# Performance work log

Hardware: AMD Instinct MI355X
Metric: run time of the kernel (lower is better)

Reference implementation:

```python
import jax, jax.numpy as jnp
import numpy as np
import math

EPS = 1e-8        # numeric guard in segment intersection (matches mmcv EPSILON)
MODE_EPS = 1e-6   # module's eps
N_BOXES = 1000000


def box2corners(box):
    # box: (B, N, 5) -> corners (B, N, 4, 2)
    cx, cy, w, h, a = [box[..., i:i + 1] for i in range(5)]
    x4 = jnp.asarray([0.5, -0.5, -0.5, 0.5], box.dtype) * w   # (B,N,4)
    y4 = jnp.asarray([-0.5, -0.5, 0.5, 0.5], box.dtype) * h
    c, s = jnp.cos(a), jnp.sin(a)
    return jnp.stack([x4 * c - y4 * s + cx, x4 * s + y4 * c + cy], axis=-1)


def box_intersection(corners1, corners2):
    # all pairwise segment intersections between edges of the two boxes
    line1 = jnp.concatenate([corners1, jnp.roll(corners1, -1, axis=2)], axis=-1)  # (B,N,4,4)
    line2 = jnp.concatenate([corners2, jnp.roll(corners2, -1, axis=2)], axis=-1)
    l1 = line1[:, :, :, None, :]  # (B,N,4,1,4)
    l2 = line2[:, :, None, :, :]  # (B,N,1,4,4)
    x1, y1, x2, y2 = l1[..., 0], l1[..., 1], l1[..., 2], l1[..., 3]
    x3, y3, x4, y4 = l2[..., 0], l2[..., 1], l2[..., 2], l2[..., 3]
    num = (y4 - y3) * (x2 - x1) - (x4 - x3) * (y2 - y1)
    den_t = (x4 - x3) * (y1 - y3) - (y4 - y3) * (x1 - x3)
    t = den_t / (num + EPS)
    t_chk = jnp.where(num == 0, -1.0, t)
    mask_t = (t_chk > 0) & (t_chk < 1)
    den_u = (x2 - x1) * (y1 - y3) - (y2 - y1) * (x1 - x3)
    u = -den_u / (num + EPS)
    u_chk = jnp.where(num == 0, -1.0, u)
    mask_u = (u_chk > 0) & (u_chk < 1)
    mask = mask_t & mask_u  # (B,N,4,4)
    pts = jnp.stack([x1 + t * (x2 - x1), y1 + t * (y2 - y1)], axis=-1)
    pts = pts * mask[..., None].astype(pts.dtype)
    return pts, mask  # (B,N,4,4,2), (B,N,4,4)


def box_in_box(corners1, corners2):
    # which corners of box1 lie inside box2 (projection test)
    a = corners2[:, :, 0:1, :]
    b = corners2[:, :, 1:2, :]
    d = corners2[:, :, 3:4, :]
    ab, ad, am = b - a, d - a, corners1 - a
    p_ab = jnp.sum(ab * am, -1) / jnp.sum(ab * ab, -1)
    p_ad = jnp.sum(ad * am, -1) / jnp.sum(ad * ad, -1)
    tol = 1e-6
    return (p_ab > -tol) & (p_ab < 1 + tol) & (p_ad > -tol) & (p_ad < 1 + tol)


def intersection_area(corners1, corners2):
    # differentiable convex-intersection area via vertex sort + shoelace
    inter_pts, inter_mask = box_intersection(corners1, corners2)
    c1_in_2 = box_in_box(corners1, corners2)
    c2_in_1 = box_in_box(corners2, corners1)
    B, N = corners1.shape[:2]
    verts = jnp.concatenate([corners1, corners2, inter_pts.reshape(B, N, 16, 2)], axis=2)  # (B,N,24,2)
    mask = jnp.concatenate([c1_in_2, c2_in_1, inter_mask.reshape(B, N, 16)], axis=2)       # (B,N,24)
    num_valid = jnp.sum(mask, axis=-1, keepdims=True).astype(verts.dtype)  # (B,N,1)
    center = jnp.sum(verts * mask[..., None], axis=2) / jnp.maximum(num_valid, 1.0)  # (B,N,2)
    v = verts - center[:, :, None, :]
    ang = jnp.where(mask, jnp.arctan2(v[..., 1], v[..., 0]), 1e7)  # invalid -> end
    order = jnp.argsort(ang, axis=-1)
    v_sorted = jnp.take_along_axis(v, order[..., None], axis=2)
    m_sorted = jnp.take_along_axis(mask, order, axis=2)
    first = v_sorted[:, :, 0:1, :]
    poly = jnp.where(m_sorted[..., None], v_sorted, first)  # pad with first vertex (closes polygon)
    nxt = jnp.roll(poly, -1, axis=2)
    cross = poly[..., 0] * nxt[..., 1] - poly[..., 1] * nxt[..., 0]
    return jnp.abs(jnp.sum(cross, axis=-1)) * 0.5  # (B,N)


def diff_iou_rotated_2d(box1, box2):
    c1, c2 = box2corners(box1), box2corners(box2)
    inter = intersection_area(c1, c2)
    area1 = box1[..., 2] * box1[..., 3]
    area2 = box2[..., 2] * box2[..., 3]
    return inter / (area1 + area2 - inter)


def obb2hbb_xyxy(obb):
    cx, cy, w, h, a = obb[:, 0], obb[:, 1], obb[:, 2], obb[:, 3], obb[:, 4]
    c, s = jnp.abs(jnp.cos(a)), jnp.abs(jnp.sin(a))
    dw = (w * c + h * s) * 0.5
    dh = (w * s + h * c) * 0.5
    return jnp.stack([cx - dw, cy - dh, cx + dw, cy + dh], axis=-1)


def setup_inputs():
    key = jax.random.key(0)
    k = jax.random.split(key, 7)
    N = N_BOXES
    cxy = jax.random.uniform(k[0], (N, 2), jnp.float32, 0.0, 1024.0)
    wh = jax.random.uniform(k[1], (N, 2), jnp.float32, 8.0, 128.0)
    ang = jax.random.uniform(k[2], (N, 1), jnp.float32, -np.pi / 2, np.pi / 2)
    pred = jnp.concatenate([cxy, wh, ang], axis=-1)
    jit_xy = jax.random.uniform(k[3], (N, 2), jnp.float32, -10.0, 10.0)
    jit_wh = jax.random.uniform(k[4], (N, 2), jnp.float32, 0.8, 1.25)
    jit_a = jax.random.uniform(k[5], (N, 1), jnp.float32, -0.3, 0.3)
    target = jnp.concatenate([pred[:, :2] + jit_xy, pred[:, 2:4] * jit_wh, pred[:, 4:5] + jit_a], axis=-1)
    weight = jax.random.uniform(k[6], (N,), jnp.float32, 0.5, 1.5)
    return {"pred": pred, "target": target, "weight": weight}


def reference(pred, target, weight):
    eps = MODE_EPS
    ious = jnp.clip(diff_iou_rotated_2d(pred[None], target[None])[0], 0.0, 1.0)  # (N,)
    # enclosing HBB for penalty terms
    hp, ht = obb2hbb_xyxy(pred), obb2hbb_xyxy(target)
    en_wh = jnp.clip(jnp.maximum(hp[:, 2:], ht[:, 2:]) - jnp.minimum(hp[:, :2], ht[:, :2]), 0.0)
    c2 = en_wh[:, 0] ** 2 + en_wh[:, 1] ** 2 + eps
    rho2 = (target[:, 0] - pred[:, 0]) ** 2 + (target[:, 1] - pred[:, 1]) ** 2
    factor = 4.0 / (math.pi ** 2)
    v = factor * (jnp.arctan(target[:, 2] / (target[:, 3] + eps)) - jnp.arctan(pred[:, 2] / (pred[:, 3] + eps))) ** 2
    alpha = jax.lax.stop_gradient((ious > 0.5).astype(v.dtype) * v / (1.0 - ious + v + eps))
    cious = ious - (jnp.clip(rho2 / c2, 0.0, 1.0) + alpha * v)
    loss = (1.0 - cious) * weight
    return jnp.mean(loss)  # loss_weight=1.0, reduction='mean'
```

## Files before the change

### kernel.cpp

```cpp
#include <hip/hip_runtime.h>
#include <math.h>


#define BLOCK 256
#define NV 16
#define PAIRS 2
#define LDS_STRIDE 17

typedef float v2f __attribute__((ext_vector_type(2)));

struct CEList {
    int n;
    unsigned char lo[128];
    unsigned char hi[128];
};

constexpr CEList make_ces16() {
    CEList L{};
    L.n = 0;
    for (int p = 1; p < NV; p <<= 1)
        for (int k = p; k >= 1; k >>= 1)
            for (int j = k % p; j + k < NV; j += 2 * k)
                for (int i = 0; i < k; i++) {
                    int lo = i + j, hi = i + j + k;
                    if (hi < NV && (lo / (2 * p)) == (hi / (2 * p))) {
                        L.lo[L.n] = (unsigned char)lo;
                        L.hi[L.n] = (unsigned char)hi;
                        L.n++;
                    }
                }
    return L;
}

constexpr CEList CES = make_ces16();

__device__ __forceinline__ float frcp(float x) {
    return __builtin_amdgcn_rcpf(x);
}

__device__ __forceinline__ v2f splat2(float x) {
    v2f r; r.x = x; r.y = x; return r;
}

__device__ __forceinline__ float hadd2(v2f v) { return v.x + v.y; }

__device__ __forceinline__ float angle_key(float x, float y) {
    float ax = fabsf(x), ay = fabsf(y);
    float den = ax + ay;
    float r = x * frcp(den);
    r = (den > 0.f) ? r : 0.f;
    return (y >= 0.f) ? (1.f - r) : (3.f + r);
}

__device__ __forceinline__ unsigned int pack_bf2(float x, float y) {
    unsigned int bx = __float_as_uint(x) + 0x8000u;
    unsigned int by = __float_as_uint(y) + 0x8000u;
    return (by & 0xFFFF0000u) | (bx >> 16);
}

__device__ __forceinline__ float atan01(float z) {
    float z2 = z * z;
    float p = -0.01172120f;
    p = p * z2 + 0.05265332f;
    p = p * z2 - 0.11643287f;
    p = p * z2 + 0.19354346f;
    p = p * z2 - 0.33262347f;
    p = p * z2 + 0.99997726f;
    return z * p;
}

__device__ __forceinline__ float pair_loss(const float* __restrict__ p,
                                           const float* __restrict__ t,
                                           float wv,
                                           unsigned int* __restrict__ myb)
{
    const float EPSf  = 1e-8f;
    const float TOLf  = 1e-6f;
    const float MEPS  = 1e-6f;
    const float PIf   = 3.14159265358979323846f;

    float pcx = p[0], pcy = p[1], pw = p[2], ph = p[3], pa = p[4];
    float tcx = t[0], tcy = t[1], tw = t[2], th = t[3], ta = t[4];

    float ca = __cosf(pa), sa = __sinf(pa);
    float cb = __cosf(ta), sb = __sinf(ta);
    v2f C1[4], C2[4];
    {
        const float xs[4] = { 0.5f, -0.5f, -0.5f, 0.5f };
        const float ys[4] = { -0.5f, -0.5f, 0.5f, 0.5f };
        v2f R1x = { ca, sa },  R1y = { -sa, cb };
        R1y.x = -sa; R1y.y = ca;
        v2f R2x = { cb, sb },  R2y = { -sb, cb };
        R2y.x = -sb; R2y.y = cb;
        v2f CT1 = { pcx, pcy }, CT2 = { tcx, tcy };
        #pragma unroll
        for (int k = 0; k < 4; k++) {
            float x4 = xs[k] * pw, y4 = ys[k] * ph;
            C1[k] = splat2(x4) * R1x + splat2(y4) * R1y + CT1;
            float x4b = xs[k] * tw, y4b = ys[k] * th;
            C2[k] = splat2(x4b) * R2x + splat2(y4b) * R2y + CT2;
        }
    }

    v2f  V[NV];
    bool msk[NV];

    {
        v2f A  = C2[0];
        v2f AB = C2[1] - A, AD = C2[3] - A;
        float rab = frcp(hadd2(AB * AB));
        float rad = frcp(hadd2(AD * AD));
        #pragma unroll
        for (int k = 0; k < 4; k++) {
            v2f AM = C1[k] - A;
            float pab = hadd2(AB * AM) * rab;
            float pad = hadd2(AD * AM) * rad;
            msk[k] = (pab > -TOLf) && (pab < 1.f + TOLf) &&
                     (pad > -TOLf) && (pad < 1.f + TOLf);
            V[k] = C1[k];
        }
    }
    {
        v2f A  = C1[0];
        v2f AB = C1[1] - A, AD = C1[3] - A;
        float rab = frcp(hadd2(AB * AB));
        float rad = frcp(hadd2(AD * AD));
        #pragma unroll
        for (int k = 0; k < 4; k++) {
            v2f AM = C2[k] - A;
            float pab = hadd2(AB * AM) * rab;
            float pad = hadd2(AD * AM) * rad;
            msk[4 + k] = (pab > -TOLf) && (pab < 1.f + TOLf) &&
                         (pad > -TOLf) && (pad < 1.f + TOLf);
            V[4 + k] = C2[k];
        }
    }
    #pragma unroll
    for (int e1 = 0; e1 < 4; e1++) {
        v2f P1 = C1[e1];
        v2f E  = C1[(e1 + 1) & 3] - P1;
        v2f  Q[4];
        bool qm[4];
        #pragma unroll
        for (int e2 = 0; e2 < 4; e2++) {
            v2f P3 = C2[e2];
            v2f F  = C2[(e2 + 1) & 3] - P3;
            float num  = F.y * E.x - F.x * E.y;
            float rnum = frcp(num + EPSf);
            v2f D = P1 - P3;
            float den_t = F.x * D.y - F.y * D.x;
            float den_u = E.x * D.y - E.y * D.x;
            float tt = den_t * rnum;
            float uu = -den_u * rnum;
            qm[e2] = (num != 0.f) && (tt > 0.f) && (tt < 1.f)
                                  && (uu > 0.f) && (uu < 1.f);
            Q[e2] = splat2(tt) * E + P1;
        }
        bool mfL = qm[0] || qm[1];
        v2f  fL  = qm[0] ? Q[0] : Q[1];
        bool msL = qm[0] && qm[1];
        bool mfR = qm[2] || qm[3];
        v2f  fR  = qm[2] ? Q[2] : Q[3];
        bool msR = qm[2] && qm[3];
        int s0 = 8 + 2 * e1, s1 = s0 + 1;
        V[s0]   = mfL ? fL : fR;
        msk[s0] = mfL || mfR;
        v2f  t2 = msL ? Q[1] : fR;
        V[s1]   = mfL ? t2 : Q[3];
        msk[s1] = msL || (mfL && mfR) || msR;
    }

    v2f s2 = { 0.f, 0.f };
    float cnt = 0.f;
    const v2f Z2 = { 0.f, 0.f };
    #pragma unroll
    for (int k = 0; k < NV; k++) {
        s2  += msk[k] ? V[k] : Z2;
        cnt += msk[k] ? 1.f : 0.f;
    }
    float rden = frcp(fmaxf(cnt, 1.f));
    v2f cen = s2 * splat2(rden);

    unsigned int ku[NV];
    #pragma unroll
    for (int k = 0; k < NV; k++) {
        v2f R = V[k] - cen;
        myb[k] = pack_bf2(R.x, R.y);
        float a = msk[k] ? angle_key(R.x, R.y) : 1e7f;
        ku[k] = (__float_as_uint(a) & 0xFFFFFFF0u) | (unsigned int)k;
    }

    #pragma unroll
    for (int c = 0; c < CES.n; c++) {
        const int lo = CES.lo[c], hi = CES.hi[c];
        unsigned int a = ku[lo], b = ku[hi];
        ku[lo] = a < b ? a : b;
        ku[hi] = a < b ? b : a;
    }

    const unsigned int VALID_LIM = 0x49742400u;
    float gx[NV], gy[NV];
    bool  gv[NV];
    #pragma unroll
    for (int k = 0; k < NV; k++) {
        unsigned int pk = myb[ku[k] & 15u];
        gx[k] = __uint_as_float(pk << 16);
        gy[k] = __uint_as_float(pk & 0xFFFF0000u);
        gv[k] = ku[k] < VALID_LIM;
    }
    float fx = gx[0], fy = gy[0];
    float cross = 0.f;
    #pragma unroll
    for (int k = 0; k < NV; k++) {
        int kn = (k + 1) % NV;
        float axv = gv[k]  ? gx[k]  : fx, ayv = gv[k]  ? gy[k]  : fy;
        float bxv = gv[kn] ? gx[kn] : fx, byv = gv[kn] ? gy[kn] : fy;
        cross += axv * byv - ayv * bxv;
    }
    float inter = fabsf(cross) * 0.5f;

    float area1 = pw * ph, area2 = tw * th;
    float iou = inter * frcp(area1 + area2 - inter);
    iou = fminf(fmaxf(iou, 0.f), 1.f);

    float cA = fabsf(ca), sA = fabsf(sa);
    float cB = fabsf(cb), sB = fabsf(sb);
    float dw1 = (pw * cA + ph * sA) * 0.5f, dh1 = (pw * sA + ph * cA) * 0.5f;
    float dw2 = (tw * cB + th * sB) * 0.5f, dh2 = (tw * sB + th * cB) * 0.5f;
    float hp0 = pcx - dw1, hp1 = pcy - dh1, hp2 = pcx + dw1, hp3 = pcy + dh1;
    float ht0 = tcx - dw2, ht1 = tcy - dh2, ht2 = tcx + dw2, ht3 = tcy + dh2;

    float enw = fmaxf(fmaxf(hp2, ht2) - fminf(hp0, ht0), 0.f);
    float enh = fmaxf(fmaxf(hp3, ht3) - fminf(hp1, ht1), 0.f);
    float c2v = enw * enw + enh * enh + MEPS;
    float rho2 = (tcx - pcx) * (tcx - pcx) + (tcy - pcy) * (tcy - pcy);

    float factor = 4.f / (PIf * PIf);
    float r1 = tw * frcp(th + MEPS);
    float r2 = pw * frcp(ph + MEPS);
    float xd = (r1 - r2) * frcp(1.f + r1 * r2);
    float axd = fabsf(xd);
    bool  big = axd > 1.f;
    float z   = big ? frcp(axd) : axd;
    float at  = atan01(z);
    float dv  = big ? ((0.5f * PIf) - at) : at;
    float v_ = factor * dv * dv;
    float alpha = (iou > 0.5f) ? v_ * frcp(1.f - iou + v_ + MEPS) : 0.f;

    float rhoterm = fminf(fmaxf(rho2 * frcp(c2v), 0.f), 1.f);
    float ciou = iou - (rhoterm + alpha * v_);
    return (1.f - ciou) * wv;
}

__global__ __launch_bounds__(BLOCK)
void obb_ciou_kernel(const float* __restrict__ pred,
                     const float* __restrict__ tgt,
                     const float* __restrict__ wgt,
                     float* __restrict__ out,
                     int N, float invN)
{
    __shared__ unsigned int slab[BLOCK * LDS_STRIDE];
    unsigned int* myb = slab + (int)threadIdx.x * LDS_STRIDE;

    int blk0 = blockIdx.x * (BLOCK * PAIRS);
    float loss = 0.f;

    #pragma unroll
    for (int u = 0; u < PAIRS; u++) {
        int i = blk0 + u * BLOCK + (int)threadIdx.x;
        if (i < N)
            loss += pair_loss(pred + (size_t)i * 5, tgt + (size_t)i * 5,
                              wgt[i], myb);
    }

    #pragma unroll
    for (int off = 32; off > 0; off >>= 1)
        loss += __shfl_down(loss, off, 64);

    __shared__ float red[BLOCK / 64];
    int wave = threadIdx.x >> 6;
    int lane = threadIdx.x & 63;
    if (lane == 0) red[wave] = loss;
    __syncthreads();
    if (threadIdx.x == 0) {
        float s = 0.f;
        #pragma unroll
        for (int w = 0; w < BLOCK / 64; w++) s += red[w];
        atomicAdd(out, s * invN);
    }
}

extern "C" void kernel_launch(void* const* d_in, const int* in_sizes, int n_in,
                              void* d_out, int out_size, void* d_ws, size_t ws_size,
                              hipStream_t stream) {
    const float* pred = (const float*)d_in[0];
    const float* tgt  = (const float*)d_in[1];
    const float* wgt  = (const float*)d_in[2];
    float* out = (float*)d_out;
    int N = in_sizes[2];

    hipMemsetAsync(out, 0, sizeof(float) * (size_t)out_size, stream);

    int grid = (N + BLOCK * PAIRS - 1) / (BLOCK * PAIRS);
    obb_ciou_kernel<<<grid, BLOCK, 0, stream>>>(pred, tgt, wgt, out, N,
                                                1.f / (float)N);
}
```

Measured before the change: 108.0 us.

## Compute intersection in pred box frame and interleave two pairs per thread

Rewrites the polygon construction in the predicted box's local frame, so box1 is axis-aligned. This turns point-in-box tests into abs comparisons and edge intersections into a single division per edge pair. It also interleaves the two pairs per thread for ILP, gives each pair its own LDS slab, and sets launch bounds to 4 blocks per CU. The trade-offs are higher register pressure and a doubled LDS footprint per block, and the changed tolerance handling could shift edge-case results slightly.

```diff
diff --git a/kernel.cpp b/kernel.cpp
--- a/kernel.cpp
+++ b/kernel.cpp
@@ -3,8 +3,8 @@
 
 
 #define BLOCK 256
+#define PAIRS 2
 #define NV 16
-#define PAIRS 2
 #define LDS_STRIDE 17
 
 typedef float v2f __attribute__((ext_vector_type(2)));
@@ -42,7 +42,10 @@
     v2f r; r.x = x; r.y = x; return r;
 }
 
-__device__ __forceinline__ float hadd2(v2f v) { return v.x + v.y; }
+__device__ __forceinline__ v2f rot_ds(v2f e, float cd, float sd) {
+    v2f sw; sw.x = e.y; sw.y = -e.x;
+    return e * splat2(cd) + sw * splat2(sd);
+}
 
 __device__ __forceinline__ float angle_key(float x, float y) {
     float ax = fabsf(x), ay = fabsf(y);
@@ -69,208 +72,275 @@
     return z * p;
 }
 
-__device__ __forceinline__ float pair_loss(const float* __restrict__ p,
-                                           const float* __restrict__ t,
-                                           float wv,
-                                           unsigned int* __restrict__ myb)
-{
-    const float EPSf  = 1e-8f;
-    const float TOLf  = 1e-6f;
-    const float MEPS  = 1e-6f;
-    const float PIf   = 3.14159265358979323846f;
-
-    float pcx = p[0], pcy = p[1], pw = p[2], ph = p[3], pa = p[4];
-    float tcx = t[0], tcy = t[1], tw = t[2], th = t[3], ta = t[4];
-
-    float ca = __cosf(pa), sa = __sinf(pa);
-    float cb = __cosf(ta), sb = __sinf(ta);
-    v2f C1[4], C2[4];
-    {
-        const float xs[4] = { 0.5f, -0.5f, -0.5f, 0.5f };
-        const float ys[4] = { -0.5f, -0.5f, 0.5f, 0.5f };
-        v2f R1x = { ca, sa },  R1y = { -sa, cb };
-        R1y.x = -sa; R1y.y = ca;
-        v2f R2x = { cb, sb },  R2y = { -sb, cb };
-        R2y.x = -sb; R2y.y = cb;
-        v2f CT1 = { pcx, pcy }, CT2 = { tcx, tcy };
-        #pragma unroll
-        for (int k = 0; k < 4; k++) {
-            float x4 = xs[k] * pw, y4 = ys[k] * ph;
-            C1[k] = splat2(x4) * R1x + splat2(y4) * R1y + CT1;
-            float x4b = xs[k] * tw, y4b = ys[k] * th;
-            C2[k] = splat2(x4b) * R2x + splat2(y4b) * R2y + CT2;
-        }
-    }
-
-    v2f  V[NV];
-    bool msk[NV];
-
-    {
-        v2f A  = C2[0];
-        v2f AB = C2[1] - A, AD = C2[3] - A;
-        float rab = frcp(hadd2(AB * AB));
-        float rad = frcp(hadd2(AD * AD));
-        #pragma unroll
-        for (int k = 0; k < 4; k++) {
-            v2f AM = C1[k] - A;
-            float pab = hadd2(AB * AM) * rab;
-            float pad = hadd2(AD * AM) * rad;
-            msk[k] = (pab > -TOLf) && (pab < 1.f + TOLf) &&
-                     (pad > -TOLf) && (pad < 1.f + TOLf);
-            V[k] = C1[k];
-        }
-    }
-    {
-        v2f A  = C1[0];
-        v2f AB = C1[1] - A, AD = C1[3] - A;
-        float rab = frcp(hadd2(AB * AB));
-        float rad = frcp(hadd2(AD * AD));
-        #pragma unroll
-        for (int k = 0; k < 4; k++) {
-            v2f AM = C2[k] - A;
-            float pab = hadd2(AB * AM) * rab;
-            float pad = hadd2(AD * AM) * rad;
-            msk[4 + k] = (pab > -TOLf) && (pab < 1.f + TOLf) &&
-                         (pad > -TOLf) && (pad < 1.f + TOLf);
-            V[4 + k] = C2[k];
-        }
-    }
-    #pragma unroll
-    for (int e1 = 0; e1 < 4; e1++) {
-        v2f P1 = C1[e1];
-        v2f E  = C1[(e1 + 1) & 3] - P1;
-        v2f  Q[4];
-        bool qm[4];
-        #pragma unroll
-        for (int e2 = 0; e2 < 4; e2++) {
-            v2f P3 = C2[e2];
-            v2f F  = C2[(e2 + 1) & 3] - P3;
-            float num  = F.y * E.x - F.x * E.y;
-            float rnum = frcp(num + EPSf);
-            v2f D = P1 - P3;
-            float den_t = F.x * D.y - F.y * D.x;
-            float den_u = E.x * D.y - E.y * D.x;
-            float tt = den_t * rnum;
-            float uu = -den_u * rnum;
-            qm[e2] = (num != 0.f) && (tt > 0.f) && (tt < 1.f)
-                                  && (uu > 0.f) && (uu < 1.f);
-            Q[e2] = splat2(tt) * E + P1;
-        }
-        bool mfL = qm[0] || qm[1];
-        v2f  fL  = qm[0] ? Q[0] : Q[1];
-        bool msL = qm[0] && qm[1];
-        bool mfR = qm[2] || qm[3];
-        v2f  fR  = qm[2] ? Q[2] : Q[3];
-        bool msR = qm[2] && qm[3];
-        int s0 = 8 + 2 * e1, s1 = s0 + 1;
-        V[s0]   = mfL ? fL : fR;
-        msk[s0] = mfL || mfR;
-        v2f  t2 = msL ? Q[1] : fR;
-        V[s1]   = mfL ? t2 : Q[3];
-        msk[s1] = msL || (mfL && mfR) || msR;
-    }
-
-    v2f s2 = { 0.f, 0.f };
-    float cnt = 0.f;
-    const v2f Z2 = { 0.f, 0.f };
-    #pragma unroll
-    for (int k = 0; k < NV; k++) {
-        s2  += msk[k] ? V[k] : Z2;
-        cnt += msk[k] ? 1.f : 0.f;
-    }
-    float rden = frcp(fmaxf(cnt, 1.f));
-    v2f cen = s2 * splat2(rden);
-
-    unsigned int ku[NV];
-    #pragma unroll
-    for (int k = 0; k < NV; k++) {
-        v2f R = V[k] - cen;
-        myb[k] = pack_bf2(R.x, R.y);
-        float a = msk[k] ? angle_key(R.x, R.y) : 1e7f;
-        ku[k] = (__float_as_uint(a) & 0xFFFFFFF0u) | (unsigned int)k;
-    }
-
-    #pragma unroll
-    for (int c = 0; c < CES.n; c++) {
-        const int lo = CES.lo[c], hi = CES.hi[c];
-        unsigned int a = ku[lo], b = ku[hi];
-        ku[lo] = a < b ? a : b;
-        ku[hi] = a < b ? b : a;
-    }
-
-    const unsigned int VALID_LIM = 0x49742400u;
-    float gx[NV], gy[NV];
-    bool  gv[NV];
-    #pragma unroll
-    for (int k = 0; k < NV; k++) {
-        unsigned int pk = myb[ku[k] & 15u];
-        gx[k] = __uint_as_float(pk << 16);
-        gy[k] = __uint_as_float(pk & 0xFFFF0000u);
-        gv[k] = ku[k] < VALID_LIM;
-    }
-    float fx = gx[0], fy = gy[0];
-    float cross = 0.f;
-    #pragma unroll
-    for (int k = 0; k < NV; k++) {
-        int kn = (k + 1) % NV;
-        float axv = gv[k]  ? gx[k]  : fx, ayv = gv[k]  ? gy[k]  : fy;
-        float bxv = gv[kn] ? gx[kn] : fx, byv = gv[kn] ? gy[kn] : fy;
-        cross += axv * byv - ayv * bxv;
-    }
-    float inter = fabsf(cross) * 0.5f;
-
-    float area1 = pw * ph, area2 = tw * th;
-    float iou = inter * frcp(area1 + area2 - inter);
-    iou = fminf(fmaxf(iou, 0.f), 1.f);
-
-    float cA = fabsf(ca), sA = fabsf(sa);
-    float cB = fabsf(cb), sB = fabsf(sb);
-    float dw1 = (pw * cA + ph * sA) * 0.5f, dh1 = (pw * sA + ph * cA) * 0.5f;
-    float dw2 = (tw * cB + th * sB) * 0.5f, dh2 = (tw * sB + th * cB) * 0.5f;
-    float hp0 = pcx - dw1, hp1 = pcy - dh1, hp2 = pcx + dw1, hp3 = pcy + dh1;
-    float ht0 = tcx - dw2, ht1 = tcy - dh2, ht2 = tcx + dw2, ht3 = tcy + dh2;
-
-    float enw = fmaxf(fmaxf(hp2, ht2) - fminf(hp0, ht0), 0.f);
-    float enh = fmaxf(fmaxf(hp3, ht3) - fminf(hp1, ht1), 0.f);
-    float c2v = enw * enw + enh * enh + MEPS;
-    float rho2 = (tcx - pcx) * (tcx - pcx) + (tcy - pcy) * (tcy - pcy);
-
-    float factor = 4.f / (PIf * PIf);
-    float r1 = tw * frcp(th + MEPS);
-    float r2 = pw * frcp(ph + MEPS);
-    float xd = (r1 - r2) * frcp(1.f + r1 * r2);
-    float axd = fabsf(xd);
-    bool  big = axd > 1.f;
-    float z   = big ? frcp(axd) : axd;
-    float at  = atan01(z);
-    float dv  = big ? ((0.5f * PIf) - at) : at;
-    float v_ = factor * dv * dv;
-    float alpha = (iou > 0.5f) ? v_ * frcp(1.f - iou + v_ + MEPS) : 0.f;
-
-    float rhoterm = fminf(fmaxf(rho2 * frcp(c2v), 0.f), 1.f);
-    float ciou = iou - (rhoterm + alpha * v_);
-    return (1.f - ciou) * wv;
-}
-
-__global__ __launch_bounds__(BLOCK)
+__global__ __launch_bounds__(BLOCK, 4)
 void obb_ciou_kernel(const float* __restrict__ pred,
                      const float* __restrict__ tgt,
                      const float* __restrict__ wgt,
                      float* __restrict__ out,
                      int N, float invN)
 {
-    __shared__ unsigned int slab[BLOCK * LDS_STRIDE];
-    unsigned int* myb = slab + (int)threadIdx.x * LDS_STRIDE;
-
-    int blk0 = blockIdx.x * (BLOCK * PAIRS);
+    const float MEPS = 1e-6f;
+    const float PIf  = 3.14159265358979323846f;
+    const float TOLm = 1.f + 2e-6f;
+
+    __shared__ unsigned int slab[PAIRS * BLOCK * LDS_STRIDE];
+    unsigned int* const mybp[2] = {
+        slab + (int)threadIdx.x * LDS_STRIDE,
+        slab + BLOCK * LDS_STRIDE + (int)threadIdx.x * LDS_STRIDE
+    };
+
+    int base = blockIdx.x * (BLOCK * PAIRS) + (int)threadIdx.x;
+
+    float pcx[2], pcy[2], pw[2], ph[2], pa[2];
+    float tcx[2], tcy[2], tw[2], th[2], ta[2];
+    float wv[2];
+    #pragma unroll
+    for (int u = 0; u < 2; u++) {
+        int i = base + u * BLOCK;
+        bool ok = i < N;
+        int ic = ok ? i : 0;
+        wv[u] = ok ? wgt[ic] : 0.f;
+        const float* p = pred + (size_t)ic * 5;
+        const float* t = tgt  + (size_t)ic * 5;
+        pcx[u] = p[0]; pcy[u] = p[1]; pw[u] = p[2]; ph[u] = p[3]; pa[u] = p[4];
+        tcx[u] = t[0]; tcy[u] = t[1]; tw[u] = t[2]; th[u] = t[3]; ta[u] = t[4];
+    }
+
+    float ca[2], sa[2], cb[2], sb[2];
+    float hw1[2], hh1[2], hw2[2], hh2[2];
+    float ddx[2], ddy[2], cd[2], sd[2];
+    v2f c2[2], A[2], B[2], C0[2], C1[2], C2c[2], C3[2];
+    #pragma unroll
+    for (int u = 0; u < 2; u++) {
+        ca[u] = __cosf(pa[u]); sa[u] = __sinf(pa[u]);
+        cb[u] = __cosf(ta[u]); sb[u] = __sinf(ta[u]);
+        hw1[u] = 0.5f * pw[u]; hh1[u] = 0.5f * ph[u];
+        hw2[u] = 0.5f * tw[u]; hh2[u] = 0.5f * th[u];
+        ddx[u] = tcx[u] - pcx[u]; ddy[u] = tcy[u] - pcy[u];
+        v2f dd;  dd.x = ddx[u];  dd.y = ddy[u];
+        v2f dds; dds.x = ddy[u]; dds.y = -ddx[u];
+        c2[u] = dd * splat2(ca[u]) + dds * splat2(sa[u]);
+        cd[u] = cb[u] * ca[u] + sb[u] * sa[u];
+        sd[u] = sb[u] * ca[u] - cb[u] * sa[u];
+        v2f axd2; axd2.x = cd[u];  axd2.y = sd[u];
+        v2f bxd2; bxd2.x = -sd[u]; bxd2.y = cd[u];
+        A[u] = splat2(hw2[u]) * axd2;
+        B[u] = splat2(hh2[u]) * bxd2;
+        v2f qpA = c2[u] + A[u], qmA = c2[u] - A[u];
+        C0[u] = qpA - B[u]; C1[u] = qmA - B[u];
+        C2c[u] = qmA + B[u]; C3[u] = qpA + B[u];
+    }
+
+    v2f  V[2][NV];
+    bool msk[2][NV];
+
+    {
+        float exl[2], exh[2], eyl[2], eyh[2], lw2[2], lh2[2];
+        #pragma unroll
+        for (int u = 0; u < 2; u++) {
+            exl[u] = -hw1[u] - c2[u].x; exh[u] = hw1[u] - c2[u].x;
+            eyl[u] = -hh1[u] - c2[u].y; eyh[u] = hh1[u] - c2[u].y;
+            lw2[u] = hw2[u] * TOLm; lh2[u] = hh2[u] * TOLm;
+        }
+        #pragma unroll
+        for (int k = 0; k < 4; k++) {
+            #pragma unroll
+            for (int u = 0; u < 2; u++) {
+                v2f e;
+                e.x = (k == 0 || k == 3) ? exh[u] : exl[u];
+                e.y = (k < 2) ? eyl[u] : eyh[u];
+                v2f duv = rot_ds(e, cd[u], sd[u]);
+                msk[u][k] = (fabsf(duv.x) < lw2[u]) && (fabsf(duv.y) < lh2[u]);
+                V[u][k].x = (k == 0 || k == 3) ? hw1[u] : -hw1[u];
+                V[u][k].y = (k < 2) ? -hh1[u] : hh1[u];
+            }
+        }
+    }
+
+    #pragma unroll
+    for (int u = 0; u < 2; u++) {
+        float lw1 = hw1[u] * TOLm, lh1 = hh1[u] * TOLm;
+        msk[u][4] = (fabsf(C0[u].x) < lw1) && (fabsf(C0[u].y) < lh1);
+        V[u][4] = C0[u];
+        msk[u][5] = (fabsf(C1[u].x) < lw1) && (fabsf(C1[u].y) < lh1);
+        V[u][5] = C1[u];
+        msk[u][6] = (fabsf(C2c[u].x) < lw1) && (fabsf(C2c[u].y) < lh1);
+        V[u][6] = C2c[u];
+        msk[u][7] = (fabsf(C3[u].x) < lw1) && (fabsf(C3[u].y) < lh1);
+        V[u][7] = C3[u];
+    }
+
+    {
+        float Sx[2][4], Sy[2][4], Dxe[2][4], Dye[2][4], iDx[2][4], iDy[2][4];
+        #pragma unroll
+        for (int u = 0; u < 2; u++) {
+            float twcd = A[u].x + A[u].x, twsd = A[u].y + A[u].y;
+            float thsd = -(B[u].x + B[u].x), thcd = B[u].y + B[u].y;
+            float rax = frcp(twcd), ray = frcp(twsd);
+            float rbx = frcp(thsd), rby = frcp(thcd);
+            Sx[u][0] = C0[u].x; Sx[u][1] = C1[u].x;
+            Sx[u][2] = C2c[u].x; Sx[u][3] = C3[u].x;
+            Sy[u][0] = C0[u].y; Sy[u][1] = C1[u].y;
+            Sy[u][2] = C2c[u].y; Sy[u][3] = C3[u].y;
+            Dxe[u][0] = -twcd; Dxe[u][1] = -thsd; Dxe[u][2] = twcd; Dxe[u][3] = thsd;
+            Dye[u][0] = -twsd; Dye[u][1] = thcd;  Dye[u][2] = twsd; Dye[u][3] = -thcd;
+            iDx[u][0] = -rax; iDx[u][1] = -rbx; iDx[u][2] = rax; iDx[u][3] = rbx;
+            iDy[u][0] = -ray; iDy[u][1] = rby;  iDy[u][2] = ray; iDy[u][3] = -rby;
+        }
+        #pragma unroll
+        for (int e1 = 0; e1 < 4; e1++) {
+            const bool horiz = (e1 == 0) || (e1 == 2);
+            float q[2][4]; bool qm[2][4];
+            #pragma unroll
+            for (int j = 0; j < 4; j++) {
+                #pragma unroll
+                for (int u = 0; u < 2; u++) {
+                    float cc  = (e1 == 0) ? -hh1[u] : (e1 == 1) ? -hw1[u]
+                              : (e1 == 2) ?  hh1[u] :  hw1[u];
+                    float lim = horiz ? hw1[u] : hh1[u];
+                    float uu = horiz ? (cc - Sy[u][j]) * iDy[u][j]
+                                     : (cc - Sx[u][j]) * iDx[u][j];
+                    float w = horiz ? fmaf(uu, Dxe[u][j], Sx[u][j])
+                                    : fmaf(uu, Dye[u][j], Sy[u][j]);
+                    qm[u][j] = (uu > -1.f) && (uu < 0.f) && (fabsf(w) < lim);
+                    q[u][j] = w;
+                }
+            }
+            #pragma unroll
+            for (int u = 0; u < 2; u++) {
+                float cc  = (e1 == 0) ? -hh1[u] : (e1 == 1) ? -hw1[u]
+                          : (e1 == 2) ?  hh1[u] :  hw1[u];
+                bool mfL = qm[u][0] || qm[u][1];
+                float fL = qm[u][0] ? q[u][0] : q[u][1];
+                bool msL = qm[u][0] && qm[u][1];
+                bool mfR = qm[u][2] || qm[u][3];
+                float fR = qm[u][2] ? q[u][2] : q[u][3];
+                bool msR = qm[u][2] && qm[u][3];
+                int s0 = 8 + 2 * e1, s1 = s0 + 1;
+                float w0 = mfL ? fL : fR;
+                msk[u][s0] = mfL || mfR;
+                float t2v = msL ? q[u][1] : fR;
+                float w1 = mfL ? t2v : q[u][3];
+                msk[u][s1] = msL || (mfL && mfR) || msR;
+                if (horiz) { V[u][s0].x = w0; V[u][s0].y = cc;
+                             V[u][s1].x = w1; V[u][s1].y = cc; }
+                else       { V[u][s0].x = cc; V[u][s0].y = w0;
+                             V[u][s1].x = cc; V[u][s1].y = w1; }
+            }
+        }
+    }
+
+    v2f s2[2]; float cnt[2];
+    #pragma unroll
+    for (int u = 0; u < 2; u++) { s2[u] = splat2(0.f); cnt[u] = 0.f; }
+    const v2f Z2 = splat2(0.f);
+    #pragma unroll
+    for (int k = 0; k < NV; k++) {
+        #pragma unroll
+        for (int u = 0; u < 2; u++) {
+            s2[u]  += msk[u][k] ? V[u][k] : Z2;
+            cnt[u] += msk[u][k] ? 1.f : 0.f;
+        }
+    }
+    v2f cen[2];
+    #pragma unroll
+    for (int u = 0; u < 2; u++)
+        cen[u] = s2[u] * splat2(frcp(fmaxf(cnt[u], 1.f)));
+
+    unsigned int ku[2][NV];
+    #pragma unroll
+    for (int k = 0; k < NV; k++) {
+        #pragma unroll
+        for (int u = 0; u < 2; u++) {
+            v2f R = V[u][k] - cen[u];
+            mybp[u][k] = pack_bf2(R.x, R.y);
+            float a = msk[u][k] ? angle_key(R.x, R.y) : 1e7f;
+            ku[u][k] = (__float_as_uint(a) & 0xFFFFFFF0u) | (unsigned int)k;
+        }
+    }
+
+    #pragma unroll
+    for (int c = 0; c < CES.n; c++) {
+        const int lo = CES.lo[c], hi = CES.hi[c];
+        #pragma unroll
+        for (int u = 0; u < 2; u++) {
+            unsigned int a = ku[u][lo], b = ku[u][hi];
+            ku[u][lo] = a < b ? a : b;
+            ku[u][hi] = a < b ? b : a;
+        }
+    }
+
+    const unsigned int VALID_LIM = 0x49742400u;
+    float sx[2][NV], sy[2][NV];
+    {
+        float gx[2][NV], gy[2][NV]; bool gv[2][NV];
+        #pragma unroll
+        for (int k = 0; k < NV; k++) {
+            #pragma unroll
+            for (int u = 0; u < 2; u++) {
+                unsigned int pk = mybp[u][ku[u][k] & 15u];
+                gx[u][k] = __uint_as_float(pk << 16);
+                gy[u][k] = __uint_as_float(pk & 0xFFFF0000u);
+                gv[u][k] = ku[u][k] < VALID_LIM;
+            }
+        }
+        #pragma unroll
+        for (int k = 0; k < NV; k++) {
+            #pragma unroll
+            for (int u = 0; u < 2; u++) {
+                sx[u][k] = gv[u][k] ? gx[u][k] : gx[u][0];
+                sy[u][k] = gv[u][k] ? gy[u][k] : gy[u][0];
+            }
+        }
+    }
+    float cross[2] = { 0.f, 0.f };
+    #pragma unroll
+    for (int k = 0; k < NV; k++) {
+        int kn = (k + 1) & (NV - 1);
+        #pragma unroll
+        for (int u = 0; u < 2; u++)
+            cross[u] += sx[u][k] * sy[u][kn] - sy[u][k] * sx[u][kn];
+    }
+
     float loss = 0.f;
-
-    #pragma unroll
-    for (int u = 0; u < PAIRS; u++) {
-        int i = blk0 + u * BLOCK + (int)threadIdx.x;
-        if (i < N)
-            loss += pair_loss(pred + (size_t)i * 5, tgt + (size_t)i * 5,
-                              wgt[i], myb);
+    #pragma unroll
+    for (int u = 0; u < 2; u++) {
+        float inter = fabsf(cross[u]) * 0.5f;
+        float area1 = pw[u] * ph[u], area2 = tw[u] * th[u];
+        float iou = inter * frcp(area1 + area2 - inter);
+        iou = fminf(fmaxf(iou, 0.f), 1.f);
+
+        float cA = fabsf(ca[u]), sA = fabsf(sa[u]);
+        float cB = fabsf(cb[u]), sB = fabsf(sb[u]);
+        float dw1 = (pw[u] * cA + ph[u] * sA) * 0.5f;
+        float dh1 = (pw[u] * sA + ph[u] * cA) * 0.5f;
+        float dw2 = (tw[u] * cB + th[u] * sB) * 0.5f;
+        float dh2 = (tw[u] * sB + th[u] * cB) * 0.5f;
+        float hp0 = pcx[u] - dw1, hp1 = pcy[u] - dh1;
+        float hp2 = pcx[u] + dw1, hp3 = pcy[u] + dh1;
+        float ht0 = tcx[u] - dw2, ht1 = tcy[u] - dh2;
+        float ht2 = tcx[u] + dw2, ht3 = tcy[u] + dh2;
+
+        float enw = fmaxf(fmaxf(hp2, ht2) - fminf(hp0, ht0), 0.f);
+        float enh = fmaxf(fmaxf(hp3, ht3) - fminf(hp1, ht1), 0.f);
+        float c2v = enw * enw + enh * enh + MEPS;
+        float rho2 = ddx[u] * ddx[u] + ddy[u] * ddy[u];
+
+        float factor = 4.f / (PIf * PIf);
+        float r1 = tw[u] * frcp(th[u] + MEPS);
+        float r2 = pw[u] * frcp(ph[u] + MEPS);
+        float xd = (r1 - r2) * frcp(1.f + r1 * r2);
+        float axd = fabsf(xd);
+        bool  big = axd > 1.f;
+        float z   = big ? frcp(axd) : axd;
+        float at  = atan01(z);
+        float dvv = big ? ((0.5f * PIf) - at) : at;
+        float v_ = factor * dvv * dvv;
+        float alpha = (iou > 0.5f) ? v_ * frcp(1.f - iou + v_ + MEPS) : 0.f;
+
+        float rhoterm = fminf(fmaxf(rho2 * frcp(c2v), 0.f), 1.f);
+        float ciou = iou - (rhoterm + alpha * v_);
+        loss += (1.f - ciou) * wv[u];
     }
 
     #pragma unroll
```

After: 130.1 us. 20.4% more time.
